# Optimization experiments

Measured on AMD Instinct MI355X. Metric: run time of the kernel, lower is better.

The kernel has to match this reference:

```python
import jax, jax.numpy as jnp
import numpy as np
import math

IMG = 640.0
SIZES = [32.0, 64.0, 128.0, 256.0]
STRIDES = [4, 8, 16, 32]
ARS = [0.5, 1.0, 2.0]
PRE_TOPK = 1000      # RPN_PRE_NMS_TOPK_TEST
POST_TOPK = 150      # RPN_POST_NMS_TOPK_TEST
NMS_THR = 0.7        # RPN_NMS_THRESHOLD
MIN_SIZE = 4.0       # MIN_BOX_SIZE
BBOX_CLAMP = math.log(1000.0 / 16.0)
ROI_OUT = 7          # ROI_OUTPUT_SIZE


def conv(x, w, b, pad):
    y = jax.lax.conv_general_dilated(x, w, (1, 1), [(pad, pad), (pad, pad)],
                                     dimension_numbers=('NCHW', 'OIHW', 'NCHW'))
    return y + b[None, :, None, None]


def level_anchors(H, W, stride, size):
    sx = (jnp.arange(W, dtype=jnp.float32) + 0.5) * stride
    sy = (jnp.arange(H, dtype=jnp.float32) + 0.5) * stride
    SY, SX = jnp.meshgrid(sy, sx, indexing='ij')
    shifts = jnp.stack([SX, SY, SX, SY], axis=-1).reshape(-1, 4)  # [H*W,4]
    base = []
    area = size * size
    for ar in ARS:
        w = math.sqrt(area / ar)
        h = ar * w
        base.append([-w / 2.0, -h / 2.0, w / 2.0, h / 2.0])
    base = jnp.asarray(base, jnp.float32)  # [3,4]
    return (shifts[:, None, :] + base[None, :, :]).reshape(-1, 4)  # [H*W*3,4]


def decode(deltas, boxes):
    w = jnp.maximum(boxes[:, 2] - boxes[:, 0], 1e-6)
    h = jnp.maximum(boxes[:, 3] - boxes[:, 1], 1e-6)
    cx = boxes[:, 0] + 0.5 * w
    cy = boxes[:, 1] + 0.5 * h
    dx, dy = deltas[:, 0], deltas[:, 1]
    dw = jnp.minimum(deltas[:, 2], BBOX_CLAMP)
    dh = jnp.minimum(deltas[:, 3], BBOX_CLAMP)
    pcx = cx + dx * w
    pcy = cy + dy * h
    pw = w * jnp.exp(dw)
    ph = h * jnp.exp(dh)
    return jnp.stack([pcx - 0.5 * pw, pcy - 0.5 * ph, pcx + 0.5 * pw, pcy + 0.5 * ph], axis=1)


def pairwise_iou(b):
    area = jnp.maximum(b[:, 2] - b[:, 0], 0) * jnp.maximum(b[:, 3] - b[:, 1], 0)
    lt = jnp.maximum(b[:, None, :2], b[None, :, :2])
    rb = jnp.minimum(b[:, None, 2:], b[None, :, 2:])
    wh = jnp.maximum(rb - lt, 0.0)
    inter = wh[..., 0] * wh[..., 1]
    return inter / jnp.maximum(area[:, None] + area[None, :] - inter, 1e-6)


def roi_align(feat, boxes, scale):
    # feat [C,H,W]; boxes [R,4] in image coords; one bilinear sample per bin center
    C, H, W = feat.shape
    b = boxes * scale
    x1, y1, x2, y2 = b[:, 0], b[:, 1], b[:, 2], b[:, 3]
    bw = jnp.maximum(x2 - x1, 1.0)
    bh = jnp.maximum(y2 - y1, 1.0)
    g = (jnp.arange(ROI_OUT, dtype=jnp.float32) + 0.5) / ROI_OUT
    px = x1[:, None] + g[None, :] * bw[:, None]   # [R,7]
    py = y1[:, None] + g[None, :] * bh[:, None]
    Y = jnp.broadcast_to(py[:, :, None], (py.shape[0], ROI_OUT, ROI_OUT))
    X = jnp.broadcast_to(px[:, None, :], (px.shape[0], ROI_OUT, ROI_OUT))
    y0f = jnp.floor(Y)
    x0f = jnp.floor(X)
    ly = Y - y0f
    lx = X - x0f
    y0 = jnp.clip(y0f, 0, H - 1).astype(jnp.int32)
    y1i = jnp.clip(y0f + 1, 0, H - 1).astype(jnp.int32)
    x0 = jnp.clip(x0f, 0, W - 1).astype(jnp.int32)
    x1i = jnp.clip(x0f + 1, 0, W - 1).astype(jnp.int32)
    f = lambda yi, xi: feat[:, yi, xi]  # [C,R,7,7]
    val = (f(y0, x0) * (1 - ly) * (1 - lx) + f(y0, x1i) * (1 - ly) * lx
           + f(y1i, x0) * ly * (1 - lx) + f(y1i, x1i) * ly * lx)
    return val.transpose(1, 0, 2, 3)  # [R,C,7,7]


def _forward(p2, p3, p4, p5, rpn_conv_w, rpn_conv_b, obj_w, obj_b, delta_w, delta_b,
             fc1_w, fc1_b, fc2_w, fc2_b, cls_w, cls_b, bbox_w, bbox_b):
    feats = [p2, p3, p4, p5]
    all_boxes, all_scores, all_lvl = [], [], []
    for lvl, (feat, stride, size) in enumerate(zip(feats, STRIDES, SIZES)):
        hid = jax.nn.relu(conv(feat, rpn_conv_w, rpn_conv_b, 1))
        obj = conv(hid, obj_w, obj_b, 0)      # [1,3,H,W]
        dlt = conv(hid, delta_w, delta_b, 0)  # [1,12,H,W]
        _, A, H, W = obj.shape
        scores = obj.transpose(0, 2, 3, 1).reshape(-1)  # [H*W*3]
        deltas = dlt.reshape(1, A, 4, H, W).transpose(0, 3, 4, 1, 2).reshape(-1, 4)
        anchors = level_anchors(H, W, stride, size)
        top_s, idx = jax.lax.top_k(scores, PRE_TOPK)
        boxes = jnp.clip(decode(deltas[idx], anchors[idx]), 0.0, IMG - 1.0)
        ww = boxes[:, 2] - boxes[:, 0]
        hh = boxes[:, 3] - boxes[:, 1]
        valid = (ww >= MIN_SIZE) & (hh >= MIN_SIZE)
        all_boxes.append(boxes)
        all_scores.append(jnp.where(valid, top_s, -1e30))
        all_lvl.append(jnp.full((PRE_TOPK,), float(lvl), jnp.float32))
    boxes = jnp.concatenate(all_boxes)   # [4000,4]
    scores = jnp.concatenate(all_scores)
    lvls = jnp.concatenate(all_lvl)
    N = boxes.shape[0]
    order = jnp.argsort(-scores)
    boxes_s = boxes[order]
    scores_s = scores[order]
    lvl_s = lvls[order]
    # batched NMS: offset per level so different levels never suppress each other
    off_boxes = boxes_s + (lvl_s * (IMG + 1.0) * 2.0)[:, None]
    iou = pairwise_iou(off_boxes)
    idx_r = jnp.arange(N)

    def body(i, keep):
        sup = (iou[i] > NMS_THR) & (idx_r > i) & keep[i]
        return keep & (~sup)

    keep = jax.lax.fori_loop(0, N, body, jnp.ones((N,), bool))
    kept_scores = jnp.where(keep, scores_s, -1e30)
    _, top_idx = jax.lax.top_k(kept_scores, POST_TOPK)
    props = boxes_s[top_idx]  # [150,4]
    # FPN level assignment (canonical formula) for ROI pooling
    pw = jnp.maximum(props[:, 2] - props[:, 0], 0.0)
    ph = jnp.maximum(props[:, 3] - props[:, 1], 0.0)
    k = jnp.clip(jnp.floor(4.0 + jnp.log2(jnp.sqrt(pw * ph) / 224.0 + 1e-6)), 2, 5)
    pooled = jnp.zeros((POST_TOPK, p2.shape[1], ROI_OUT, ROI_OUT), props.dtype)
    for lvl, (feat, stride) in enumerate(zip(feats, STRIDES)):
        pl = roi_align(feat[0], props, 1.0 / stride)
        pooled = pooled + jnp.where((k == (lvl + 2))[:, None, None, None], pl, 0.0)
    x = pooled.reshape(POST_TOPK, -1)            # [150, 12544]
    x = jax.nn.relu(x @ fc1_w.T + fc1_b)
    x = jax.nn.relu(x @ fc2_w.T + fc2_b)
    cls = x @ cls_w.T + cls_b                    # [150, 21]
    bbx = x @ bbox_w.T + bbox_b                  # [150, 84]
    return jnp.concatenate([cls, bbx], axis=-1)  # [150, 105]


def setup_inputs() -> dict:
    key = jax.random.key(0)
    ks = jax.random.split(key, 14)
    C = 256
    rn = lambda k, shape, s: jax.random.normal(k, shape, jnp.float32) * s
    return {
        'p2': rn(ks[0], (1, C, 160, 160), 0.5),
        'p3': rn(ks[1], (1, C, 80, 80), 0.5),
        'p4': rn(ks[2], (1, C, 40, 40), 0.5),
        'p5': rn(ks[3], (1, C, 20, 20), 0.5),
        'rpn_conv_w': rn(ks[4], (C, C, 3, 3), 0.01),
        'rpn_conv_b': jnp.zeros((C,), jnp.float32),
        'obj_w': rn(ks[5], (3, C, 1, 1), 0.01),
        'obj_b': jnp.zeros((3,), jnp.float32),
        'delta_w': rn(ks[6], (12, C, 1, 1), 0.01),
        'delta_b': jnp.zeros((12,), jnp.float32),
        'fc1_w': rn(ks[7], (1024, C * ROI_OUT * ROI_OUT), 0.01),
        'fc1_b': jnp.zeros((1024,), jnp.float32),
        'fc2_w': rn(ks[8], (1024, 1024), 0.01),
        'fc2_b': jnp.zeros((1024,), jnp.float32),
        'cls_w': rn(ks[9], (21, 1024), 0.01),
        'cls_b': jnp.zeros((21,), jnp.float32),
        'bbox_w': rn(ks[10], (84, 1024), 0.001),
        'bbox_b': jnp.zeros((84,), jnp.float32),
    }


def reference(p2, p3, p4, p5, rpn_conv_w, rpn_conv_b, obj_w, obj_b, delta_w, delta_b,
              fc1_w, fc1_b, fc2_w, fc2_b, cls_w, cls_b, bbox_w, bbox_b):
    return _forward(p2, p3, p4, p5, rpn_conv_w, rpn_conv_b, obj_w, obj_b, delta_w, delta_b,
                    fc1_w, fc1_b, fc2_w, fc2_b, cls_w, cls_b, bbox_w, bbox_b)
```

## Files before the change

kernel.cpp:

```cpp
#include <hip/hip_runtime.h>
#include <cstdint>

typedef unsigned long long u64;
typedef unsigned int u32;

__device__ inline u32 fmono(float f){ u32 u = __float_as_uint(f); u32 m = (u & 0x80000000u) ? 0xFFFFFFFFu : 0x80000000u; return u ^ m; }

__device__ const int    g_H[4]       = {160, 80, 40, 20};
__device__ const int    g_strideI[4] = {4, 8, 16, 32};
__device__ const float  g_size[4]    = {32.f, 64.f, 128.f, 256.f};
__device__ const int    g_cofs[4]    = {0, 76800, 96000, 100800};
__device__ const int    g_cnt[4]     = {76800, 19200, 4800, 1200};
__device__ const int    c_blkBase[5] = {0, 1600, 2000, 2288, 2416};
__device__ const int    c_S[4]       = {4, 4, 8, 8};
__device__ const int    c_pofs[4]    = {0, 25600, 32000, 33600};
__device__ const size_t c_partofs[4] = {0, 26214400, 32768000, 36044800};

__global__ __launch_bounds__(256) void wtr_k(const float* __restrict__ w, float* __restrict__ wT){
  __shared__ float tile[32][33];
  int tx = threadIdx.x & 31, ty = threadIdx.x >> 5;
  int row0 = blockIdx.x*32, co0 = blockIdx.y*32;
  #pragma unroll
  for (int r=0;r<4;r++){
    int co = co0 + ty + r*8;
    tile[ty+r*8][tx] = w[(size_t)co*2304 + row0 + tx];
  }
  __syncthreads();
  #pragma unroll
  for (int r=0;r<4;r++){
    int row = row0 + ty + r*8;
    wT[(size_t)row*256 + co0 + tx] = tile[tx][ty+r*8];
  }
}

__global__ void wcat_k(const float* __restrict__ cls_w, const float* __restrict__ cls_b,
                       const float* __restrict__ bbox_w, const float* __restrict__ bbox_b,
                       float* __restrict__ wcat, float* __restrict__ bcat){
  int t = blockIdx.x*256 + threadIdx.x;
  if (t < 105*1024){ int o = t >> 10, k = t & 1023; wcat[t] = (o < 21) ? cls_w[o*1024+k] : bbox_w[(o-21)*1024+k]; }
  if (t < 105) bcat[t] = (t < 21) ? cls_b[t] : bbox_b[t-21];
}

#define KC 4
__global__ __launch_bounds__(256) void rpn_conv_all_k(
    const float* __restrict__ p0, const float* __restrict__ p1,
    const float* __restrict__ p2f, const float* __restrict__ p3f,
    const float* __restrict__ wT, float* __restrict__ convp)
{
  int bid = blockIdx.x;
  int lvl = (bid >= c_blkBase[1]) + (bid >= c_blkBase[2]) + (bid >= c_blkBase[3]);
  int local = bid - c_blkBase[lvl];
  int nz  = c_S[lvl];
  int H = g_H[lvl], W = H;
  const float* in = (lvl==0)?p0:((lvl==1)?p1:((lvl==2)?p2f:p3f));
  float* part = convp + c_partofs[lvl];
  int zb   = local % nz;
  int cb   = (local / nz) & 3;
  int tile = local / (nz*4);

  int tilesX = (W + 15) >> 4;
  int tr0 = (tile / tilesX) * 16;
  int tc0 = (tile % tilesX) * 16;
  int ciPer = 256 / nz;
  int ciBeg = zb * ciPer;
  int t   = threadIdx.x;
  int tco = t & 15, tp = t >> 4;
  int pr = (tp >> 2) * 4, pc = (tp & 3) * 4;
  int HW = H*W;

  __shared__ float sIn[KC][18][20];
  __shared__ float sW[KC*9][64];

  float* sInF = &sIn[0][0][0];
  float* sWF  = &sW[0][0];

  int   iOff[6]; int iLds[6]; bool iOk[6];
  #pragma unroll
  for (int s=0;s<6;s++){
    int e = t + s*256;
    bool a = (s<5) || (t < (KC*324 - 5*256));
    int ee = a ? e : 0;
    int c = ee/324, r2 = ee%324, row = r2/18, col = r2%18;
    int gy = tr0+row-1, gx = tc0+col-1;
    bool ok = a && ((unsigned)gy < (unsigned)H) && ((unsigned)gx < (unsigned)W);
    iOff[s] = c*HW + gy*W + gx;
    iLds[s] = c*360 + row*20 + col;
    iOk[s]  = ok;
  }
  bool iAct5 = (t < (KC*324 - 5*256));
  int wOff[3]; int wLds[3];
  #pragma unroll
  for (int s=0;s<3;s++){
    int e4 = t + s*256;
    bool a = (s<2) || (t < (KC*9*16 - 2*256));
    int ee = a ? e4 : 0;
    int row = ee>>4, c4 = (ee&15)<<2;
    wOff[s] = row*256 + cb*64 + c4;
    wLds[s] = row*64 + c4;
  }
  bool wAct2 = (t < (KC*9*16 - 2*256));

  float acc[4][16];
  #pragma unroll
  for (int o=0;o<4;o++)
    #pragma unroll
    for (int p=0;p<16;p++) acc[o][p]=0.f;

  float  ri0,ri1,ri2,ri3,ri4,ri5;
  float4 rw0,rw1,rw2;

  {
    const float* inb = in + (size_t)ciBeg*HW;
    const float* wb  = wT + (size_t)ciBeg*2304;
    ri0 = iOk[0] ? inb[iOff[0]] : 0.f;
    ri1 = iOk[1] ? inb[iOff[1]] : 0.f;
    ri2 = iOk[2] ? inb[iOff[2]] : 0.f;
    ri3 = iOk[3] ? inb[iOff[3]] : 0.f;
    ri4 = iOk[4] ? inb[iOff[4]] : 0.f;
    ri5 = iOk[5] ? inb[iOff[5]] : 0.f;
    rw0 = *(const float4*)&wb[wOff[0]];
    rw1 = *(const float4*)&wb[wOff[1]];
    if (wAct2) rw2 = *(const float4*)&wb[wOff[2]];
  }

  int ciEnd = ciBeg + ciPer;
  for (int ci0=ciBeg; ci0<ciEnd; ci0+=KC){
    sInF[iLds[0]] = ri0; sInF[iLds[1]] = ri1; sInF[iLds[2]] = ri2;
    sInF[iLds[3]] = ri3; sInF[iLds[4]] = ri4;
    if (iAct5) sInF[iLds[5]] = ri5;
    *(float4*)&sWF[wLds[0]] = rw0;
    *(float4*)&sWF[wLds[1]] = rw1;
    if (wAct2) *(float4*)&sWF[wLds[2]] = rw2;
    __syncthreads();

    if (ci0 + KC < ciEnd){
      const float* inb = in + (size_t)(ci0+KC)*HW;
      const float* wb  = wT + (size_t)(ci0+KC)*2304;
      ri0 = iOk[0] ? inb[iOff[0]] : 0.f;
      ri1 = iOk[1] ? inb[iOff[1]] : 0.f;
      ri2 = iOk[2] ? inb[iOff[2]] : 0.f;
      ri3 = iOk[3] ? inb[iOff[3]] : 0.f;
      ri4 = iOk[4] ? inb[iOff[4]] : 0.f;
      ri5 = iOk[5] ? inb[iOff[5]] : 0.f;
      rw0 = *(const float4*)&wb[wOff[0]];
      rw1 = *(const float4*)&wb[wOff[1]];
      if (wAct2) rw2 = *(const float4*)&wb[wOff[2]];
    }

    #pragma unroll
    for (int c=0;c<KC;c++){
      float rin[6][6];
      #pragma unroll
      for (int rr=0;rr<6;rr++){
        float4 a = *(const float4*)&sIn[c][pr+rr][pc];
        float2 b = *(const float2*)&sIn[c][pr+rr][pc+4];
        rin[rr][0]=a.x; rin[rr][1]=a.y; rin[rr][2]=a.z; rin[rr][3]=a.w;
        rin[rr][4]=b.x; rin[rr][5]=b.y;
      }
      #pragma unroll
      for (int k=0;k<9;k++){
        int ky=k/3, kx=k%3;
        float4 w0 = *(const float4*)&sW[c*9+k][tco*4];
        float wv[4] = {w0.x,w0.y,w0.z,w0.w};
        #pragma unroll
        for (int dr=0;dr<4;dr++)
          #pragma unroll
          for (int dc=0;dc<4;dc++){
            float iv = rin[dr+ky][dc+kx];
            int p = dr*4+dc;
            #pragma unroll
            for (int o=0;o<4;o++) acc[o][p] = fmaf(wv[o], iv, acc[o][p]);
          }
      }
    }
    __syncthreads();
  }

  int coBase = cb*64 + tco*4;
  float* pb = part + (size_t)zb*HW*256;
  #pragma unroll
  for (int dr=0;dr<4;dr++){
    int gy = tr0+pr+dr; if (gy>=H) continue;
    #pragma unroll
    for (int dc=0;dc<4;dc++){
      int gx = tc0+pc+dc; if (gx>=W) continue;
      int p = dr*4+dc;
      *(float4*)&pb[(size_t)(gy*W+gx)*256 + coBase] = make_float4(acc[0][p],acc[1][p],acc[2][p],acc[3][p]);
    }
  }
}

__global__ __launch_bounds__(256) void rpn_heads_k(
  const float* __restrict__ convp, const float* __restrict__ cbias,
  const float* __restrict__ ow, const float* __restrict__ ob,
  const float* __restrict__ dw, const float* __restrict__ db,
  float* __restrict__ scores, float* __restrict__ deltas)
{
  __shared__ float sw[15][256];
  int t = threadIdx.x;
  for (int e=t; e<15*256; e+=256){ int o=e>>8, k=e&255; sw[o][k] = (o<3)? ow[o*256+k] : dw[(o-3)*256+k]; }
  __syncthreads();
  int wv = t>>6, lane = t&63;
  float4 bv = *(const float4*)&cbias[lane*4];
  #pragma unroll
  for (int i=0;i<16;i++){
    int gpx = blockIdx.x*64 + wv*16 + i;
    if (gpx >= 34000) return;
    int lvl = (gpx >= 25600) + (gpx >= 32000) + (gpx >= 33600);
    int S = c_S[lvl];
    size_t stride = (size_t)g_H[lvl]*g_H[lvl]*256;
    const float* pb = convp + c_partofs[lvl] + (size_t)(gpx - c_pofs[lvl])*256 + lane*4;
    float vx=0.f, vy=0.f, vz=0.f, vw=0.f;
    for (int s=0;s<S;s++){
      float4 q = *(const float4*)(pb + (size_t)s*stride);
      vx += q.x; vy += q.y; vz += q.z; vw += q.w;
    }
    vx += bv.x; vy += bv.y; vz += bv.z; vw += bv.w;
    vx = vx>0.f?vx:0.f; vy = vy>0.f?vy:0.f; vz = vz>0.f?vz:0.f; vw = vw>0.f?vw:0.f;
    float a[15];
    #pragma unroll
    for (int o=0;o<15;o++){
      const float* w = &sw[o][lane*4];
      a[o] = w[0]*vx + w[1]*vy + w[2]*vz + w[3]*vw;
    }
    #pragma unroll
    for (int off=32; off; off>>=1)
      #pragma unroll
      for (int o=0;o<15;o++) a[o] += __shfl_xor(a[o], off, 64);
    if (lane==0){
      for (int q=0;q<3;q++) scores[gpx*3+q] = a[q] + ob[q];
      for (int q=0;q<3;q++)
        for (int j=0;j<4;j++)
          deltas[(size_t)(gpx*3+q)*4 + j] = a[3+q*4+j] + db[q*4+j];
    }
  }
}

__global__ __launch_bounds__(1024) void topk_k(
  const float* __restrict__ scores, float* __restrict__ top_s, u32* __restrict__ top_idx)
{
  int lvl = blockIdx.x;
  int base = g_cofs[lvl], N = g_cnt[lvl];
  const int K = 1000;
  __shared__ u32 hist[4096];
  __shared__ u64 sbuf[4096];
  __shared__ u32 shThr; __shared__ int scnt;
  u32* scratch = (u32*)sbuf;
  int t = threadIdx.x;
  for (int e=t; e<4096; e+=1024) hist[e]=0;
  __syncthreads();
  for (int e=t; e<N; e+=1024){
    u32 m = fmono(scores[base+e]);
    atomicAdd(&hist[m>>20], 1u);
  }
  __syncthreads();
  {
    u32* src = hist; u32* dst = scratch;
    for (int off=1; off<4096; off<<=1){
      for (int i=t;i<4096;i+=1024){
        u32 v = src[i];
        if (i+off < 4096) v += src[i+off];
        dst[i] = v;
      }
      __syncthreads();
      u32* tmp = src; src = dst; dst = tmp;
    }
    for (int i=t;i<4096;i+=1024){
      u32 s0 = src[i];
      if (s0 >= (u32)K && (i==4095 || src[i+1] < (u32)K)) shThr = (u32)i;
    }
    if (t==0) scnt = 0;
    __syncthreads();
  }
  u32 thr = shThr;
  for (int e=t; e<4096; e+=1024) sbuf[e]=0ull;
  __syncthreads();
  for (int e=t; e<N; e+=1024){
    u32 m = fmono(scores[base+e]);
    if ((m>>20) >= thr){
      int p = atomicAdd(&scnt, 1);
      if (p < 4096) sbuf[p] = ((u64)m << 32) | (u32)(~(u32)e);
    }
  }
  __syncthreads();
  for (int k=2;k<=4096;k<<=1)
    for (int j=k>>1;j>0;j>>=1){
      for (int i=t;i<4096;i+=1024){
        int ixj = i^j;
        if (ixj > i){
          u64 x = sbuf[i], y = sbuf[ixj];
          bool up = ((i & k) == 0);
          bool swp = up ? (x<y) : (x>y);
          if (swp){ sbuf[i]=y; sbuf[ixj]=x; }
        }
      }
      __syncthreads();
    }
  if (t<K){
    u64 key = sbuf[t];
    u32 idx = ~((u32)key);
    top_idx[lvl*1000+t] = idx;
    top_s[lvl*1000+t]   = scores[base + (int)idx];
  }
}

__global__ __launch_bounds__(1024) void sort_k(const u32* __restrict__ top_idx, const float* __restrict__ top_s,
  const float* __restrict__ deltas,
  float* __restrict__ cat_sc, float4* __restrict__ cat_bx,
  float* __restrict__ scores_s, float4* __restrict__ boxes_s, float4* __restrict__ obox)
{
  int t = threadIdx.x;
  for (int e=t; e<4000; e+=1024){
    int lvl = e/1000;
    u32 idx = top_idx[e];
    float score = top_s[e];
    int W = g_H[lvl];
    int strd = g_strideI[lvl];
    float size = g_size[lvl];
    int a = (int)(idx % 3u); int pix = (int)(idx / 3u);
    int px = pix % W, py = pix / W;
    double area = (double)size*(double)size;
    double ar = (a==0)?0.5:((a==1)?1.0:2.0);
    double wd = sqrt(area/ar);
    double hd = ar*wd;
    float bx1 = (float)(-wd*0.5), by1 = (float)(-hd*0.5), bx2=(float)(wd*0.5), by2=(float)(hd*0.5);
    float sx = ((float)px + 0.5f)*(float)strd;
    float sy = ((float)py + 0.5f)*(float)strd;
    float ax1 = sx+bx1, ay1=sy+by1, ax2=sx+bx2, ay2=sy+by2;
    float w = fmaxf(ax2-ax1, 1e-6f), h = fmaxf(ay2-ay1, 1e-6f);
    float cx = ax1 + 0.5f*w, cy = ay1 + 0.5f*h;
    const float* d = &deltas[(size_t)(g_cofs[lvl] + (int)idx)*4];
    float dx = d[0], dy = d[1];
    float dwv = fminf(d[2], 4.135166556742356f);
    float dhv = fminf(d[3], 4.135166556742356f);
    float pcx = cx + dx*w, pcy = cy + dy*h;
    float pw = w*expf(dwv), ph = h*expf(dhv);
    float x1 = pcx - 0.5f*pw, y1 = pcy - 0.5f*ph, x2 = pcx + 0.5f*pw, y2 = pcy + 0.5f*ph;
    x1 = fminf(fmaxf(x1,0.f),639.f); y1 = fminf(fmaxf(y1,0.f),639.f);
    x2 = fminf(fmaxf(x2,0.f),639.f); y2 = fminf(fmaxf(y2,0.f),639.f);
    bool valid = ((x2-x1) >= 4.f) && ((y2-y1) >= 4.f);
    cat_bx[e] = make_float4(x1,y1,x2,y2);
    cat_sc[e] = valid ? score : -1e30f;
  }
  __syncthreads();
  __shared__ u64 s[4096];
  for (int i=t;i<4096;i+=1024){
    u64 key = 0;
    if (i<4000) key = ((u64)fmono(cat_sc[i])<<32) | (u32)(~(u32)i);
    s[i]=key;
  }
  __syncthreads();
  for (int k=2;k<=4096;k<<=1)
    for (int j=k>>1;j>0;j>>=1){
      for (int i=t;i<4096;i+=1024){
        int ixj=i^j;
        if (ixj>i){
          u64 x=s[i], y=s[ixj];
          bool up = ((i&k)==0);
          bool swp = up ? (x<y):(x>y);
          if (swp){ s[i]=y; s[ixj]=x; }
        }
      }
      __syncthreads();
    }
  for (int r=t;r<4000;r+=1024){
    u32 o = ~((u32)s[r]);
    float4 b = cat_bx[o];
    scores_s[r] = cat_sc[o];
    boxes_s[r] = b;
    float off = (float)(o/1000u) * 1282.0f;
    obox[r] = make_float4(b.x+off, b.y+off, b.z+off, b.w+off);
  }
}

__global__ __launch_bounds__(256) void iou_k(const float4* __restrict__ obox, u64* __restrict__ mask)
{
  int w = threadIdx.x;
  int i = blockIdx.x*4 + threadIdx.y;
  if (i >= 4000 || w >= 63) return;
  float4 bi = obox[i];
  float ai = fmaxf(bi.z-bi.x,0.f)*fmaxf(bi.w-bi.y,0.f);
  u64 bits=0;
  int c0=w*64;
  for (int l=0;l<64;l++){
    int c=c0+l;
    if (c>=4000) break;
    if (c<=i) continue;
    float4 bc = obox[c];
    float ac = fmaxf(bc.z-bc.x,0.f)*fmaxf(bc.w-bc.y,0.f);
    float ltx = fmaxf(bi.x, bc.x), lty = fmaxf(bi.y, bc.y);
    float rbx = fminf(bi.z, bc.z), rby = fminf(bi.w, bc.w);
    float wx = fmaxf(rbx-ltx,0.f), wy = fmaxf(rby-lty,0.f);
    float inter = wx*wy;
    float uni = fmaxf(ai+ac-inter, 1e-6f);
    if (inter/uni > 0.7f) bits |= (1ull<<l);
  }
  mask[(size_t)i*63 + w] = bits;
}

__global__ __launch_bounds__(64) void nms_scan_k(const u64* __restrict__ mask,
   const float* __restrict__ scores_s, const float4* __restrict__ boxes_s, float4* __restrict__ props)
{
  int lane = threadIdx.x;
  bool act = lane < 63;
  const u64* mrow = mask + lane;
  u64 removed = 0;

  const int NG = 63;
  u64 bufA[64], bufB[64];
  #pragma unroll
  for (int j=0;j<64;j++){
    int i = j;
    bufA[j] = (act && i < 4000) ? mrow[(size_t)i*63] : 0ull;
  }

  for (int g=0; g<NG; g+=2){
    if (g+1 < NG){
      #pragma unroll
      for (int j=0;j<64;j++){
        int i = (g+1)*64 + j;
        bufB[j] = (act && i < 4000) ? mrow[(size_t)i*63] : 0ull;
      }
    }
    {
      u64 rm = removed, kb = 0;
      #pragma unroll
      for (int j=0;j<64;j++){
        u64 bit = 1ull<<j;
        bool keep = ((rm & bit) == 0ull);
        if (keep){ kb |= bit; rm |= bufA[j]; }
      }
      kb = __shfl(kb, g, 64);
      #pragma unroll
      for (int j=0;j<64;j++){
        if ((kb >> j) & 1ull) removed |= bufA[j];
      }
    }
    if (g+2 < NG){
      #pragma unroll
      for (int j=0;j<64;j++){
        int i = (g+2)*64 + j;
        bufA[j] = (act && i < 4000) ? mrow[(size_t)i*63] : 0ull;
      }
    }
    if (g+1 < NG){
      u64 rm = removed, kb = 0;
      #pragma unroll
      for (int j=0;j<64;j++){
        u64 bit = 1ull<<j;
        bool keep = ((rm & bit) == 0ull);
        if (keep){ kb |= bit; rm |= bufB[j]; }
      }
      kb = __shfl(kb, g+1, 64);
      #pragma unroll
      for (int j=0;j<64;j++){
        if ((kb >> j) & 1ull) removed |= bufB[j];
      }
    }
  }

  u64 keepbits = ~removed;
  u64 selbits = 0;
  if (act){
    #pragma unroll
    for (int j=0;j<64;j++){
      int i = lane*64 + j;
      if (i < 4000 && ((keepbits>>j)&1ull) && scores_s[i] > -1e29f) selbits |= (1ull<<j);
    }
  }
  u64 validbits = 0;
  if (act){
    int nvalid = 4000 - lane*64;
    if (nvalid >= 64) validbits = ~0ull;
    else if (nvalid > 0) validbits = (1ull<<nvalid) - 1ull;
  }
  u64 nonbits = (~selbits) & validbits;

  int cntSel = __popcll(selbits);
  int incS = cntSel;
  #pragma unroll
  for (int off2=1; off2<64; off2<<=1){ int v = __shfl_up(incS, off2, 64); if (lane>=off2) incS += v; }
  int exSel = incS - cntSel;
  int totalSel = __shfl(incS, 63, 64);
  int cnt = totalSel < 150 ? totalSel : 150;

  int cntNon = __popcll(nonbits);
  int incN = cntNon;
  #pragma unroll
  for (int off2=1; off2<64; off2<<=1){ int v = __shfl_up(incN, off2, 64); if (lane>=off2) incN += v; }
  int exNon = incN - cntNon;

  if (act){
    int r = exSel;
    #pragma unroll
    for (int j=0;j<64;j++){
      if ((selbits>>j)&1ull){
        if (r < 150) props[r] = boxes_s[lane*64 + j];
        r++;
      }
    }
    int r2 = cnt + exNon;
    #pragma unroll
    for (int j=0;j<64;j++){
      if ((nonbits>>j)&1ull){
        if (r2 < 150) props[r2] = boxes_s[lane*64 + j];
        r2++;
      }
    }
  }
}

__global__ __launch_bounds__(256) void roi_k(const float* __restrict__ p2, const float* __restrict__ p3,
  const float* __restrict__ p4, const float* __restrict__ p5, const float4* __restrict__ props, float* __restrict__ x0)
{
  int roi = blockIdx.y, p = blockIdx.x, c = threadIdx.x;
  float4 b = props[roi];
  float pw = fmaxf(b.z-b.x, 0.f), ph = fmaxf(b.w-b.y, 0.f);
  float kf = floorf(4.f + log2f(sqrtf(pw*ph)/224.f + 1e-6f));
  kf = fminf(fmaxf(kf, 2.f), 5.f);
  int lvl = (int)kf - 2;
  const float* f = (lvl==0)?p2:((lvl==1)?p3:((lvl==2)?p4:p5));
  int H = g_H[lvl]; int HW = H*H;
  float scale = 1.f/(float)g_strideI[lvl];
  float x1 = b.x*scale, y1 = b.y*scale, x2 = b.z*scale, y2 = b.w*scale;
  float bw = fmaxf(x2-x1, 1.f), bh = fmaxf(y2-y1, 1.f);
  int py = p/7, px = p%7;
  float gx = ((float)px + 0.5f)/7.f;
  float gy = ((float)py + 0.5f)/7.f;
  float X = x1 + gx*bw;
  float Y = y1 + gy*bh;
  float x0f = floorf(X), y0f = floorf(Y);
  float lx = X - x0f, ly = Y - y0f;
  int xi0 = (int)fminf(fmaxf(x0f,0.f),(float)(H-1));
  int xi1 = (int)fminf(fmaxf(x0f+1.f,0.f),(float)(H-1));
  int yi0 = (int)fminf(fmaxf(y0f,0.f),(float)(H-1));
  int yi1 = (int)fminf(fmaxf(y0f+1.f,0.f),(float)(H-1));
  float v00 = f[(size_t)c*HW + yi0*H + xi0];
  float v01 = f[(size_t)c*HW + yi0*H + xi1];
  float v10 = f[(size_t)c*HW + yi1*H + xi0];
  float v11 = f[(size_t)c*HW + yi1*H + xi1];
  float val = v00*(1.f-ly)*(1.f-lx) + v01*(1.f-ly)*lx + v10*ly*(1.f-lx) + v11*ly*lx;
  x0[(size_t)roi*12544 + c*49 + p] = val;
}

__global__ __launch_bounds__(256) void fc_split_k(const float* __restrict__ X, const float* __restrict__ Wt,
  float* __restrict__ partial, int M, int N, int K, int KS)
{
  __shared__ float sx[32][33];
  __shared__ float sw[32][64];
  int t = threadIdx.x;
  int tn = t & 15, tm = t >> 4;
  int nb = blockIdx.x, mb = blockIdx.y, zb = blockIdx.z;
  int row0 = mb*32 + tm*2, col0 = nb*64 + tn*4;
  int kbeg = zb*KS, kend = kbeg + KS;
  float acc[2][4] = {{0,0,0,0},{0,0,0,0}};
  int wn = t & 63, kg = t >> 6;
  for (int k0=kbeg;k0<kend;k0+=32){
    for (int e=t;e<1024;e+=256){
      int m=e>>5, kk=e&31;
      int row=mb*32+m;
      sx[m][kk] = (row<M)? X[(size_t)row*K + k0+kk] : 0.f;
    }
    int co = nb*64+wn;
    if (co<N){
      const float* wp = &Wt[(size_t)co*K + k0 + kg*8];
      float4 va = *(const float4*)wp;
      float4 vb = *(const float4*)(wp+4);
      sw[kg*8+0][wn]=va.x; sw[kg*8+1][wn]=va.y; sw[kg*8+2][wn]=va.z; sw[kg*8+3][wn]=va.w;
      sw[kg*8+4][wn]=vb.x; sw[kg*8+5][wn]=vb.y; sw[kg*8+6][wn]=vb.z; sw[kg*8+7][wn]=vb.w;
    } else {
      #pragma unroll
      for (int j=0;j<8;j++) sw[kg*8+j][wn]=0.f;
    }
    __syncthreads();
    #pragma unroll 8
    for (int kk=0;kk<32;kk++){
      float xa = sx[tm*2+0][kk], xb = sx[tm*2+1][kk];
      float4 wv = *(const float4*)&sw[kk][tn*4];
      acc[0][0]=fmaf(xa,wv.x,acc[0][0]); acc[0][1]=fmaf(xa,wv.y,acc[0][1]);
      acc[0][2]=fmaf(xa,wv.z,acc[0][2]); acc[0][3]=fmaf(xa,wv.w,acc[0][3]);
      acc[1][0]=fmaf(xb,wv.x,acc[1][0]); acc[1][1]=fmaf(xb,wv.y,acc[1][1]);
      acc[1][2]=fmaf(xb,wv.z,acc[1][2]); acc[1][3]=fmaf(xb,wv.w,acc[1][3]);
    }
    __syncthreads();
  }
  for (int dm=0;dm<2;dm++){
    int row=row0+dm; if (row>=M) continue;
    for (int dn=0;dn<4;dn++){
      int col=col0+dn; if (col>=N) continue;
      partial[((size_t)zb*M + row)*N + col] = acc[dm][dn];
    }
  }
}

__global__ __launch_bounds__(256) void fc_reduce_k(const float* __restrict__ partial, const float* __restrict__ bias,
  float* __restrict__ Y, int M, int N, int S, int dorelu)
{
  int idx = blockIdx.x*256 + threadIdx.x;
  if (idx >= M*N) return;
  int col = idx % N;
  float v = bias[col];
  size_t stride = (size_t)M*N;
  for (int s=0;s<S;s++) v += partial[s*stride + idx];
  if (dorelu) v = fmaxf(v, 0.f);
  Y[idx] = v;
}

extern "C" void kernel_launch(void* const* d_in, const int* in_sizes, int n_in,
                              void* d_out, int out_size, void* d_ws, size_t ws_size,
                              hipStream_t stream)
{
  (void)in_sizes; (void)n_in; (void)out_size; (void)ws_size;
  const float* p[4] = {(const float*)d_in[0], (const float*)d_in[1], (const float*)d_in[2], (const float*)d_in[3]};
  const float* rpn_w = (const float*)d_in[4];
  const float* rpn_b = (const float*)d_in[5];
  const float* obj_w = (const float*)d_in[6];
  const float* obj_b = (const float*)d_in[7];
  const float* del_w = (const float*)d_in[8];
  const float* del_b = (const float*)d_in[9];
  const float* fc1_w = (const float*)d_in[10];
  const float* fc1_b = (const float*)d_in[11];
  const float* fc2_w = (const float*)d_in[12];
  const float* fc2_b = (const float*)d_in[13];
  const float* cls_w = (const float*)d_in[14];
  const float* cls_b = (const float*)d_in[15];
  const float* bbox_w= (const float*)d_in[16];
  const float* bbox_b= (const float*)d_in[17];

  char* ws = (char*)d_ws;
  size_t off = 0;
  auto alloc = [&](size_t bytes){ size_t o = off; off += (bytes + 255) & ~(size_t)255; return o; };
  float*  wT1      = (float*)(ws + alloc(589824ull*4));
  float*  hid      = (float*)(ws + alloc(34000ull*256*4));
  float*  scores   = (float*)(ws + alloc(102000ull*4));
  float*  deltas   = (float*)(ws + alloc(102000ull*16));
  float*  top_s    = (float*)(ws + alloc(4000ull*4));
  u32*    top_idx  = (u32*)  (ws + alloc(4000ull*4));
  float*  cat_sc   = (float*)(ws + alloc(4000ull*4));
  float4* cat_bx   = (float4*)(ws + alloc(4000ull*16));
  float*  scores_s = (float*)(ws + alloc(4000ull*4));
  float4* boxes_s  = (float4*)(ws + alloc(4000ull*16));
  float4* obox     = (float4*)(ws + alloc(4000ull*16));
  u64*    mask     = (u64*)  (ws + alloc(4000ull*63*8));
  float4* props    = (float4*)(ws + alloc(150ull*16));
  float*  x0       = (float*)(ws + alloc(150ull*12544*4));
  float*  x1       = (float*)(ws + alloc(150ull*1024*4));
  float*  x2       = (float*)(ws + alloc(150ull*1024*4));
  float*  wcat     = (float*)(ws + alloc(105ull*1024*4));
  float*  bcat     = (float*)(ws + alloc(105ull*4));
  float*  convp    = (float*)(ws + alloc(36864000ull*4));
  float*  partial  = hid;

  hipLaunchKernelGGL(wtr_k, dim3(72,8), dim3(256), 0, stream, rpn_w, wT1);
  hipLaunchKernelGGL(wcat_k, dim3((105*1024+255)/256), dim3(256), 0, stream, cls_w, cls_b, bbox_w, bbox_b, wcat, bcat);

  hipLaunchKernelGGL(rpn_conv_all_k, dim3(2416), dim3(256), 0, stream,
                     p[0], p[1], p[2], p[3], wT1, convp);

  hipLaunchKernelGGL(rpn_heads_k, dim3((34000+63)/64), dim3(256), 0, stream,
                     convp, rpn_b, obj_w, obj_b, del_w, del_b, scores, deltas);
  hipLaunchKernelGGL(topk_k, dim3(4), dim3(1024), 0, stream, scores, top_s, top_idx);
  hipLaunchKernelGGL(sort_k, dim3(1), dim3(1024), 0, stream, top_idx, top_s, deltas,
                     cat_sc, cat_bx, scores_s, boxes_s, obox);
  hipLaunchKernelGGL(iou_k, dim3(1000), dim3(64,4), 0, stream, obox, mask);
  hipLaunchKernelGGL(nms_scan_k, dim3(1), dim3(64), 0, stream, mask, scores_s, boxes_s, props);
  hipLaunchKernelGGL(roi_k, dim3(49,150), dim3(256), 0, stream, p[0],p[1],p[2],p[3], props, x0);

  hipLaunchKernelGGL(fc_split_k, dim3(16,5,28), dim3(256), 0, stream, x0, fc1_w, partial, 150, 1024, 12544, 448);
  hipLaunchKernelGGL(fc_reduce_k, dim3((150*1024+255)/256), dim3(256), 0, stream, partial, fc1_b, x1, 150, 1024, 28, 1);
  hipLaunchKernelGGL(fc_split_k, dim3(16,5,8), dim3(256), 0, stream, x1, fc2_w, partial, 150, 1024, 1024, 128);
  hipLaunchKernelGGL(fc_reduce_k, dim3((150*1024+255)/256), dim3(256), 0, stream, partial, fc2_b, x2, 150, 1024, 8, 1);
  hipLaunchKernelGGL(fc_split_k, dim3(2,5,8), dim3(256), 0, stream, x2, wcat, partial, 150, 105, 1024, 128);
  hipLaunchKernelGGL(fc_reduce_k, dim3((150*105+255)/256), dim3(256), 0, stream, partial, bcat, (float*)d_out, 150, 105, 8, 0);
}
```

Measured before the change: 1.181 ms.

## Double-buffer RPN conv shared memory and merge weight prep kernels

```diff
diff --git a/kernel.cpp b/kernel.cpp
--- a/kernel.cpp
+++ b/kernel.cpp
@@ -16,29 +16,32 @@
 __device__ const int    c_pofs[4]    = {0, 25600, 32000, 33600};
 __device__ const size_t c_partofs[4] = {0, 26214400, 32768000, 36044800};
 
-__global__ __launch_bounds__(256) void wtr_k(const float* __restrict__ w, float* __restrict__ wT){
-  __shared__ float tile[32][33];
-  int tx = threadIdx.x & 31, ty = threadIdx.x >> 5;
-  int row0 = blockIdx.x*32, co0 = blockIdx.y*32;
-  #pragma unroll
-  for (int r=0;r<4;r++){
-    int co = co0 + ty + r*8;
-    tile[ty+r*8][tx] = w[(size_t)co*2304 + row0 + tx];
-  }
-  __syncthreads();
-  #pragma unroll
-  for (int r=0;r<4;r++){
-    int row = row0 + ty + r*8;
-    wT[(size_t)row*256 + co0 + tx] = tile[tx][ty+r*8];
-  }
-}
-
-__global__ void wcat_k(const float* __restrict__ cls_w, const float* __restrict__ cls_b,
-                       const float* __restrict__ bbox_w, const float* __restrict__ bbox_b,
-                       float* __restrict__ wcat, float* __restrict__ bcat){
-  int t = blockIdx.x*256 + threadIdx.x;
-  if (t < 105*1024){ int o = t >> 10, k = t & 1023; wcat[t] = (o < 21) ? cls_w[o*1024+k] : bbox_w[(o-21)*1024+k]; }
-  if (t < 105) bcat[t] = (t < 21) ? cls_b[t] : bbox_b[t-21];
+__global__ __launch_bounds__(256) void prep_k(const float* __restrict__ w, float* __restrict__ wT,
+  const float* __restrict__ cls_w, const float* __restrict__ cls_b,
+  const float* __restrict__ bbox_w, const float* __restrict__ bbox_b,
+  float* __restrict__ wcat, float* __restrict__ bcat)
+{
+  int b = blockIdx.x;
+  if (b < 576){
+    __shared__ float tile[32][33];
+    int tx = threadIdx.x & 31, ty = threadIdx.x >> 5;
+    int row0 = (b % 72)*32, co0 = (b / 72)*32;
+    #pragma unroll
+    for (int r=0;r<4;r++){
+      int co = co0 + ty + r*8;
+      tile[ty+r*8][tx] = w[(size_t)co*2304 + row0 + tx];
+    }
+    __syncthreads();
+    #pragma unroll
+    for (int r=0;r<4;r++){
+      int row = row0 + ty + r*8;
+      wT[(size_t)row*256 + co0 + tx] = tile[tx][ty+r*8];
+    }
+  } else {
+    int t = (b-576)*256 + threadIdx.x;
+    if (t < 105*1024){ int o = t >> 10, k = t & 1023; wcat[t] = (o < 21) ? cls_w[o*1024+k] : bbox_w[(o-21)*1024+k]; }
+    if (t < 105) bcat[t] = (t < 21) ? cls_b[t] : bbox_b[t-21];
+  }
 }
 
 #define KC 4
@@ -68,11 +71,8 @@
   int pr = (tp >> 2) * 4, pc = (tp & 3) * 4;
   int HW = H*W;
 
-  __shared__ float sIn[KC][18][20];
-  __shared__ float sW[KC*9][64];
-
-  float* sInF = &sIn[0][0][0];
-  float* sWF  = &sW[0][0];
+  __shared__ float sIn[2][KC][18][20];
+  __shared__ float sW[2][KC*9][64];
 
   int   iOff[6]; int iLds[6]; bool iOk[6];
   #pragma unroll
@@ -121,19 +121,22 @@
     rw0 = *(const float4*)&wb[wOff[0]];
     rw1 = *(const float4*)&wb[wOff[1]];
     if (wAct2) rw2 = *(const float4*)&wb[wOff[2]];
-  }
-
-  int ciEnd = ciBeg + ciPer;
-  for (int ci0=ciBeg; ci0<ciEnd; ci0+=KC){
+    float* sInF = &sIn[0][0][0][0];
+    float* sWF  = &sW[0][0][0];
     sInF[iLds[0]] = ri0; sInF[iLds[1]] = ri1; sInF[iLds[2]] = ri2;
     sInF[iLds[3]] = ri3; sInF[iLds[4]] = ri4;
     if (iAct5) sInF[iLds[5]] = ri5;
     *(float4*)&sWF[wLds[0]] = rw0;
     *(float4*)&sWF[wLds[1]] = rw1;
     if (wAct2) *(float4*)&sWF[wLds[2]] = rw2;
-    __syncthreads();
-
-    if (ci0 + KC < ciEnd){
+  }
+  __syncthreads();
+
+  int ciEnd = ciBeg + ciPer;
+  int cur = 0;
+  for (int ci0=ciBeg; ci0<ciEnd; ci0+=KC){
+    bool more = (ci0 + KC < ciEnd);
+    if (more){
       const float* inb = in + (size_t)(ci0+KC)*HW;
       const float* wb  = wT + (size_t)(ci0+KC)*2304;
       ri0 = iOk[0] ? inb[iOff[0]] : 0.f;
@@ -147,33 +150,49 @@
       if (wAct2) rw2 = *(const float4*)&wb[wOff[2]];
     }
 
-    #pragma unroll
-    for (int c=0;c<KC;c++){
-      float rin[6][6];
-      #pragma unroll
-      for (int rr=0;rr<6;rr++){
-        float4 a = *(const float4*)&sIn[c][pr+rr][pc];
-        float2 b = *(const float2*)&sIn[c][pr+rr][pc+4];
-        rin[rr][0]=a.x; rin[rr][1]=a.y; rin[rr][2]=a.z; rin[rr][3]=a.w;
-        rin[rr][4]=b.x; rin[rr][5]=b.y;
-      }
-      #pragma unroll
-      for (int k=0;k<9;k++){
-        int ky=k/3, kx=k%3;
-        float4 w0 = *(const float4*)&sW[c*9+k][tco*4];
-        float wv[4] = {w0.x,w0.y,w0.z,w0.w};
+    {
+      const float (*sInB)[18][20] = sIn[cur];
+      const float (*sWB)[64] = sW[cur];
+      #pragma unroll
+      for (int c=0;c<KC;c++){
+        float rin[6][6];
         #pragma unroll
-        for (int dr=0;dr<4;dr++)
+        for (int rr=0;rr<6;rr++){
+          float4 a = *(const float4*)&sInB[c][pr+rr][pc];
+          float2 b = *(const float2*)&sInB[c][pr+rr][pc+4];
+          rin[rr][0]=a.x; rin[rr][1]=a.y; rin[rr][2]=a.z; rin[rr][3]=a.w;
+          rin[rr][4]=b.x; rin[rr][5]=b.y;
+        }
+        #pragma unroll
+        for (int k=0;k<9;k++){
+          int ky=k/3, kx=k%3;
+          float4 w0 = *(const float4*)&sWB[c*9+k][tco*4];
+          float wv[4] = {w0.x,w0.y,w0.z,w0.w};
           #pragma unroll
-          for (int dc=0;dc<4;dc++){
-            float iv = rin[dr+ky][dc+kx];
-            int p = dr*4+dc;
+          for (int dr=0;dr<4;dr++)
             #pragma unroll
-            for (int o=0;o<4;o++) acc[o][p] = fmaf(wv[o], iv, acc[o][p]);
-          }
-      }
+            for (int dc=0;dc<4;dc++){
+              float iv = rin[dr+ky][dc+kx];
+              int p = dr*4+dc;
+              #pragma unroll
+              for (int o=0;o<4;o++) acc[o][p] = fmaf(wv[o], iv, acc[o][p]);
+            }
+        }
+      }
+    }
+
+    if (more){
+      float* sInF = &sIn[cur^1][0][0][0];
+      float* sWF  = &sW[cur^1][0][0];
+      sInF[iLds[0]] = ri0; sInF[iLds[1]] = ri1; sInF[iLds[2]] = ri2;
+      sInF[iLds[3]] = ri3; sInF[iLds[4]] = ri4;
+      if (iAct5) sInF[iLds[5]] = ri5;
+      *(float4*)&sWF[wLds[0]] = rw0;
+      *(float4*)&sWF[wLds[1]] = rw1;
+      if (wAct2) *(float4*)&sWF[wLds[2]] = rw2;
     }
     __syncthreads();
+    cur ^= 1;
   }
 
   int coBase = cb*64 + tco*4;
@@ -651,8 +670,8 @@
   float*  convp    = (float*)(ws + alloc(36864000ull*4));
   float*  partial  = hid;
 
-  hipLaunchKernelGGL(wtr_k, dim3(72,8), dim3(256), 0, stream, rpn_w, wT1);
-  hipLaunchKernelGGL(wcat_k, dim3((105*1024+255)/256), dim3(256), 0, stream, cls_w, cls_b, bbox_w, bbox_b, wcat, bcat);
+  hipLaunchKernelGGL(prep_k, dim3(996), dim3(256), 0, stream,
+                     rpn_w, wT1, cls_w, cls_b, bbox_w, bbox_b, wcat, bcat);
 
   hipLaunchKernelGGL(rpn_conv_all_k, dim3(2416), dim3(256), 0, stream,
                      p[0], p[1], p[2], p[3], wT1, convp);
```

New measurement: 1.321 ms. 1.12x slower.
